# Optimization experiments

Measured on AMD Instinct MI355X. Metric: run time of the kernel, lower is better.

The kernel has to match this reference:

```python
import jax, jax.numpy as jnp
import numpy as np

NEG_INF = float(np.finfo(np.float32).min)
B, KLEN, QLEN, KDIM, QDIM, ADIM, H = 2, 2048, 2048, 512, 512, 512, 8
D_K = ADIM // H


def setup_inputs() -> dict:
    key = jax.random.key(0)
    ks = jax.random.split(key, 12)
    s = 0.05  # param init scale
    inp = {
        "key_in": jax.random.normal(ks[0], (B, KLEN, KDIM), jnp.float32),
        "value_in": jax.random.normal(ks[1], (B, KLEN, KDIM), jnp.float32),
        "query_in": jax.random.normal(ks[2], (B, QLEN, QDIM), jnp.float32),
        "Wk": jax.random.normal(ks[3], (KDIM, ADIM), jnp.float32) * s,
        "bk": jax.random.normal(ks[4], (ADIM,), jnp.float32) * s,
        "Wv": jax.random.normal(ks[5], (KDIM, ADIM), jnp.float32) * s,
        "bv": jax.random.normal(ks[6], (ADIM,), jnp.float32) * s,
        "Wq": jax.random.normal(ks[7], (QDIM, ADIM), jnp.float32) * s,
        "bq": jax.random.normal(ks[8], (ADIM,), jnp.float32) * s,
        "Wo": jax.random.normal(ks[9], (ADIM, KDIM), jnp.float32) * s,
        "bo": jax.random.normal(ks[10], (KDIM,), jnp.float32) * s,
    }
    # key-length padding mask, [B, qlen, klen]; 0 = masked
    klens = jnp.array([KLEN, KLEN - 512], jnp.int32)
    valid = (jnp.arange(KLEN)[None, :] < klens[:, None]).astype(jnp.int32)  # [B, klen]
    inp["mask"] = jnp.broadcast_to(valid[:, None, :], (B, QLEN, KLEN))
    return inp


def reference(key_in, value_in, query_in, Wk, bk, Wv, bv, Wq, bq, Wo, bo, mask):
    # projections -> [B, L, H, d_k]
    k = (key_in @ Wk + bk).reshape(B, KLEN, H, D_K)
    v = (value_in @ Wv + bv).reshape(B, KLEN, H, D_K)
    q = (query_in @ Wq + bq).reshape(B, QLEN, H, D_K)
    # scaled dot-product scores [B, H, qlen, klen]
    e = jnp.einsum('bqhd,bkhd->bhqk', q, k) / jnp.sqrt(jnp.float32(D_K))
    e = jnp.where(mask[:, None, :, :] == 0, NEG_INF, e)
    aw = jax.nn.softmax(e, axis=-1)  # dropout p=0.0 -> identity
    cv = jnp.einsum('bhqk,bkhd->bqhd', aw, v).reshape(B, QLEN, ADIM)
    cv = cv @ Wo + bo  # [B, qlen, kdim]
    return cv, aw
```

## Files before the change

kernel.cpp:

```cpp
#include <hip/hip_runtime.h>

typedef short sh8 __attribute__((ext_vector_type(8)));
typedef float fx4 __attribute__((ext_vector_type(4)));
typedef float fl4 __attribute__((ext_vector_type(4)));
typedef unsigned short us4 __attribute__((ext_vector_type(4)));

__device__ __forceinline__ unsigned short f2bf(float f) {
    union { float f; unsigned u; } v; v.f = f;
    unsigned r = v.u + 0x7FFFu + ((v.u >> 16) & 1u);
    return (unsigned short)(r >> 16);
}
__device__ __forceinline__ unsigned pk2(float a, float b) {
    return (unsigned)f2bf(a) | ((unsigned)f2bf(b) << 16);
}
__device__ __forceinline__ void gl16(const unsigned short* g, unsigned short* l) {
    __builtin_amdgcn_global_load_lds(
        (const __attribute__((address_space(1))) unsigned int*)g,
        (__attribute__((address_space(3))) unsigned int*)l, 16, 0, 0);
}

__global__ __launch_bounds__(256) void prep(const float* __restrict__ w0,
                                            const float* __restrict__ w1,
                                            const float* __restrict__ w2,
                                            const float* __restrict__ w3,
                                            const int* __restrict__ mask,
                                            unsigned short* __restrict__ wt,
                                            unsigned long long* __restrict__ mp2) {
    __shared__ float tw[32][33];
    const int bid = blockIdx.x, tid = threadIdx.x;
    if (bid < 1024) {
        const int t = bid;
        const int z = t >> 8, bx = t & 15, by = (t >> 4) & 15;
        const float* W = z == 0 ? w0 : z == 1 ? w1 : z == 2 ? w2 : w3;
        unsigned short* Wt = wt + (size_t)z * 262144;
        const int tx = tid & 31, ty = tid >> 5;
        #pragma unroll
        for (int i = 0; i < 4; ++i)
            tw[ty + i * 8][tx] = W[(size_t)(by * 32 + ty + i * 8) * 512 + bx * 32 + tx];
        __syncthreads();
        #pragma unroll
        for (int i = 0; i < 4; ++i)
            Wt[(size_t)(bx * 32 + ty + i * 8) * 512 + by * 32 + tx] = f2bf(tw[tx][ty + i * 8]);
    } else {
        const int p = bid - 1024;
        const int b = p >> 3, k = (p & 7) * 256 + tid;
        int v = mask[(size_t)b * 4194304 + k];
        unsigned long long bal = __ballot(v != 0);
        if ((tid & 63) == 0) mp2[b * 32 + (k >> 6)] = bal;
    }
}

template <int MODE>
__global__ __launch_bounds__(256) void gemm_k(const unsigned short* __restrict__ Abf,
                                              const float* __restrict__ xk,
                                              const float* __restrict__ xv,
                                              const float* __restrict__ xq,
                                              const unsigned short* __restrict__ Wtall,
                                              const float* __restrict__ b0,
                                              const float* __restrict__ b1,
                                              const float* __restrict__ b2,
                                              void* __restrict__ outp,
                                              unsigned short* __restrict__ VtB) {
    const int z = blockIdx.z;
    const float* Afp = (MODE == 0) ? (z == 0 ? xk : (z == 1 ? xv : xq)) : nullptr;
    const unsigned short* Bt = Wtall + (size_t)z * (512 * 512);
    const float* bias = (MODE == 0) ? (z == 0 ? b0 : (z == 1 ? b1 : b2)) : b0;

    __shared__ __align__(16) unsigned short As[128 * 64];
    __shared__ __align__(16) unsigned short Bs[64 * 64];

    const int tid = threadIdx.x;
    const int wid = tid >> 6, lane = tid & 63, lr = lane & 15, lg = lane >> 4;
    const int wr = wid >> 1, wc = wid & 1;
    const int mblk = blockIdx.x * 128, nblk = blockIdx.y * 64;
    const int r7 = lr & 7;

    fx4 acc[4][2];
    #pragma unroll
    for (int mf = 0; mf < 4; ++mf)
        #pragma unroll
        for (int nf = 0; nf < 2; ++nf)
            #pragma unroll
            for (int j = 0; j < 4; ++j) acc[mf][nf][j] = 0.f;

    for (int kt = 0; kt < 8; ++kt) {
        __syncthreads();
        if (MODE == 0) {
            #pragma unroll
            for (int g = 0; g < 4; ++g) {
                int ci = g * 256 + tid;
                int r = ci >> 3, c = ci & 7;
                const float* src = Afp + (size_t)(mblk + r) * 512 + kt * 64 + c * 8;
                float4 v0 = *(const float4*)(src);
                float4 v1 = *(const float4*)(src + 4);
                union { unsigned short u[8]; sh8 v; } pk;
                pk.u[0] = f2bf(v0.x); pk.u[1] = f2bf(v0.y);
                pk.u[2] = f2bf(v0.z); pk.u[3] = f2bf(v0.w);
                pk.u[4] = f2bf(v1.x); pk.u[5] = f2bf(v1.y);
                pk.u[6] = f2bf(v1.z); pk.u[7] = f2bf(v1.w);
                *(sh8*)&As[r * 64 + ((c ^ (r & 7)) * 8)] = pk.v;
            }
        } else {
            #pragma unroll
            for (int g = 0; g < 4; ++g) {
                int ci = wid * 256 + g * 64 + lane;
                int r = ci >> 3, c = (ci & 7) ^ (r & 7);
                gl16(Abf + (size_t)(mblk + r) * 512 + kt * 64 + c * 8, &As[(wid * 256 + g * 64) * 8]);
            }
        }
        #pragma unroll
        for (int g = 0; g < 2; ++g) {
            int ci = wid * 128 + g * 64 + lane;
            int r = ci >> 3, c = (ci & 7) ^ (r & 7);
            gl16(Bt + (size_t)(nblk + r) * 512 + kt * 64 + c * 8, &Bs[(wid * 128 + g * 64) * 8]);
        }
        __syncthreads();
        #pragma unroll
        for (int d = 0; d < 2; ++d) {
            sh8 af[4], bf[2];
            #pragma unroll
            for (int mf = 0; mf < 4; ++mf)
                af[mf] = *(const sh8*)&As[(wr * 64 + mf * 16 + lr) * 64 + (((d * 4 + lg) ^ r7) * 8)];
            #pragma unroll
            for (int nf = 0; nf < 2; ++nf)
                bf[nf] = *(const sh8*)&Bs[(wc * 32 + nf * 16 + lr) * 64 + (((d * 4 + lg) ^ r7) * 8)];
            #pragma unroll
            for (int mf = 0; mf < 4; ++mf)
                #pragma unroll
                for (int nf = 0; nf < 2; ++nf)
                    acc[mf][nf] = __builtin_amdgcn_mfma_f32_16x16x32_bf16(af[mf], bf[nf], acc[mf][nf], 0, 0, 0);
        }
    }

    if (MODE == 0 && z == 1) {
        #pragma unroll
        for (int nf = 0; nf < 2; ++nf) {
            int n = nblk + wc * 32 + nf * 16 + lr;
            float bv = bias[n];
            int h = n >> 6, dd = n & 63;
            #pragma unroll
            for (int mf = 0; mf < 4; ++mf) {
                int m0 = mblk + wr * 64 + mf * 16 + lg * 4;
                int bb = m0 >> 11, lq = m0 & 2047;
                ushort4 o;
                o.x = f2bf(acc[mf][nf][0] + bv);
                o.y = f2bf(acc[mf][nf][1] + bv);
                o.z = f2bf(acc[mf][nf][2] + bv);
                o.w = f2bf(acc[mf][nf][3] + bv);
                *(ushort4*)(VtB + ((size_t)(bb * 8 + h) * 64 + dd) * 2048 + lq) = o;
            }
        }
    } else {
        #pragma unroll
        for (int nf = 0; nf < 2; ++nf) {
            int n = nblk + wc * 32 + nf * 16 + lr;
            float bv = bias[n];
            #pragma unroll
            for (int mf = 0; mf < 4; ++mf) {
                #pragma unroll
                for (int j = 0; j < 4; ++j) {
                    int m = mblk + wr * 64 + mf * 16 + lg * 4 + j;
                    float val = acc[mf][nf][j] + bv;
                    if (MODE == 0) {
                        if (z == 2) val *= 0.125f;
                        int bb = m >> 11, lq = m & 2047, h = n >> 6, dd = n & 63;
                        ((unsigned short*)outp)[(size_t)(((z * 2 + bb) * 8 + h) * 2048 + lq) * 64 + dd] = f2bf(val);
                    } else {
                        ((float*)outp)[(size_t)m * 512 + n] = val;
                    }
                }
            }
        }
    }
}

__device__ __forceinline__ void stage_k1(const unsigned short* Kg, unsigned short* sK,
                                         int t, int w, int lane) {
    #pragma unroll
    for (int g = 0; g < 2; ++g) {
        int ci = w * 128 + g * 64 + lane;
        int r = ci >> 3, c = (ci & 7) ^ (r & 7);
        gl16(Kg + (size_t)(t * 64 + r) * 64 + c * 8, sK + (w * 128 + g * 64) * 8);
    }
}
__device__ __forceinline__ void stage_kv(const unsigned short* Kg, const unsigned short* Vg,
                                         unsigned short* sK, unsigned short* sV,
                                         int t, int w, int lane) {
    #pragma unroll
    for (int g = 0; g < 2; ++g) {
        int ci = w * 128 + g * 64 + lane;
        int r = ci >> 3, c = (ci & 7) ^ (r & 7);
        gl16(Kg + (size_t)(t * 64 + r) * 64 + c * 8, sK + (w * 128 + g * 64) * 8);
        gl16(Vg + (size_t)r * 2048 + t * 64 + c * 8, sV + (w * 128 + g * 64) * 8);
    }
}

__global__ __launch_bounds__(256, 2) void attn_fused(const unsigned short* __restrict__ qkv,
                                                     const unsigned short* __restrict__ Vt,
                                                     const unsigned long long* __restrict__ mp2,
                                                     float* __restrict__ aw,
                                                     unsigned short* __restrict__ cv) {
    const int bid = blockIdx.x;
    const int swz = (bid & 7) * 64 + (bid >> 3);
    const int qb = swz & 31, bh = swz >> 5;
    const int b = bh >> 3, h = bh & 7;
    const unsigned short* Kg = qkv + (size_t)bh * 131072;
    const unsigned short* Vg = Vt + (size_t)bh * 131072;
    const unsigned short* Qg = qkv + 2 * 2097152 + (size_t)bh * 131072 + (size_t)qb * 4096;

    __shared__ __align__(16) unsigned short Ks[2][4096];
    __shared__ __align__(16) unsigned short Vs[2][4096];
    __shared__ __align__(16) unsigned short Pb[4096];

    const int tid = threadIdx.x, w = tid >> 6, lane = tid & 63, lr = lane & 15, lg = lane >> 4;
    const int r7 = lr & 7;
    const int q = qb * 64 + w * 16 + lr;

    sh8 qf0 = *(const sh8*)(Qg + (w * 16 + lr) * 64 + lg * 8);
    sh8 qf1 = *(const sh8*)(Qg + (w * 16 + lr) * 64 + 32 + lg * 8);
    unsigned long long mwv = (lane < 32) ? mp2[b * 32 + lane] : 0ull;

    float m_ = -3e38f, l_ = 0.f;
    asm volatile("s_waitcnt vmcnt(0)" ::: "memory");
    stage_k1(Kg, Ks[0], 0, w, lane);
    stage_k1(Kg, Ks[1], 1, w, lane);
    for (int kt = 0; kt < 32; ++kt) {
        if (kt >= 1 && kt <= 30)
            stage_k1(Kg, Ks[(kt + 1) & 1], kt + 1, w, lane);
        if (kt == 31) asm volatile("s_waitcnt vmcnt(0)" ::: "memory");
        else          asm volatile("s_waitcnt vmcnt(2)" ::: "memory");
        asm volatile("s_barrier" ::: "memory");
        unsigned long long mw = __shfl(mwv, kt, 64);
        if (mw != 0ull) {
            const unsigned short* KsB = Ks[kt & 1];
            fx4 accs[4];
            #pragma unroll
            for (int mt = 0; mt < 4; ++mt) {
                sh8 kf0 = *(const sh8*)&KsB[(mt * 16 + lr) * 64 + ((lg ^ r7) * 8)];
                sh8 kf1 = *(const sh8*)&KsB[(mt * 16 + lr) * 64 + (((4 + lg) ^ r7) * 8)];
                fx4 zz; zz[0] = 0.f; zz[1] = 0.f; zz[2] = 0.f; zz[3] = 0.f;
                zz = __builtin_amdgcn_mfma_f32_16x16x32_bf16(kf0, qf0, zz, 0, 0, 0);
                accs[mt] = __builtin_amdgcn_mfma_f32_16x16x32_bf16(kf1, qf1, zz, 0, 0, 0);
            }
            float sv[16], tmax = -3e38f;
            if (mw == ~0ull) {
                #pragma unroll
                for (int mt = 0; mt < 4; ++mt)
                    #pragma unroll
                    for (int j = 0; j < 4; ++j) {
                        float s = accs[mt][j];
                        sv[mt * 4 + j] = s; tmax = fmaxf(tmax, s);
                    }
            } else {
                #pragma unroll
                for (int mt = 0; mt < 4; ++mt)
                    #pragma unroll
                    for (int j = 0; j < 4; ++j) {
                        int kl = mt * 16 + lg * 4 + j;
                        bool ok = (mw >> kl) & 1ull;
                        float s = ok ? accs[mt][j] : -3e38f;
                        sv[mt * 4 + j] = s; tmax = fmaxf(tmax, s);
                    }
            }
            float mnew = fmaxf(m_, tmax);
            float ps = 0.f;
            #pragma unroll
            for (int i = 0; i < 16; ++i) ps += __expf(sv[i] - mnew);
            l_ = l_ * __expf(m_ - mnew) + ps;
            m_ = mnew;
        }
        asm volatile("s_barrier" ::: "memory");
    }
    #pragma unroll
    for (int off = 16; off <= 32; off <<= 1) {
        float mo = __shfl_xor(m_, off), lo = __shfl_xor(l_, off);
        float mn = fmaxf(m_, mo);
        l_ = l_ * __expf(m_ - mn) + lo * __expf(mo - mn);
        m_ = mn;
    }
    const float M = (l_ > 0.f) ? m_ : 0.f;
    const float rinv = (l_ > 0.f) ? 1.f / l_ : 0.f;

    fx4 acco[4];
    #pragma unroll
    for (int md = 0; md < 4; ++md) { acco[md][0] = 0.f; acco[md][1] = 0.f; acco[md][2] = 0.f; acco[md][3] = 0.f; }
    float* awb = aw + (size_t)bh * 4194304 + (size_t)q * 2048;

    asm volatile("s_waitcnt vmcnt(0)" ::: "memory");
    stage_kv(Kg, Vg, Ks[0], Vs[0], 0, w, lane);
    stage_kv(Kg, Vg, Ks[1], Vs[1], 1, w, lane);

    for (int kt = 0; kt < 32; ++kt) {
        if (kt >= 1 && kt <= 30)
            stage_kv(Kg, Vg, Ks[(kt + 1) & 1], Vs[(kt + 1) & 1], kt + 1, w, lane);
        if (kt == 0 || kt == 31) asm volatile("s_waitcnt vmcnt(4)" ::: "memory");
        else                     asm volatile("s_waitcnt vmcnt(8)" ::: "memory");
        asm volatile("s_barrier" ::: "memory");

        unsigned long long mw = __shfl(mwv, kt, 64);
        const unsigned short* KsB = Ks[kt & 1];
        const unsigned short* VsB = Vs[kt & 1];

        if (mw != 0ull) {
            fx4 accs[4];
            #pragma unroll
            for (int mt = 0; mt < 4; ++mt) {
                sh8 kf0 = *(const sh8*)&KsB[(mt * 16 + lr) * 64 + ((lg ^ r7) * 8)];
                sh8 kf1 = *(const sh8*)&KsB[(mt * 16 + lr) * 64 + (((4 + lg) ^ r7) * 8)];
                fx4 zz; zz[0] = 0.f; zz[1] = 0.f; zz[2] = 0.f; zz[3] = 0.f;
                zz = __builtin_amdgcn_mfma_f32_16x16x32_bf16(kf0, qf0, zz, 0, 0, 0);
                accs[mt] = __builtin_amdgcn_mfma_f32_16x16x32_bf16(kf1, qf1, zz, 0, 0, 0);
            }
            bool full = (mw == ~0ull);
            #pragma unroll
            for (int mt = 0; mt < 4; ++mt) {
                fl4 pw;
                #pragma unroll
                for (int j = 0; j < 4; ++j) {
                    int kl = mt * 16 + lg * 4 + j;
                    bool ok = full || ((mw >> kl) & 1ull);
                    float p = ok ? __expf(accs[mt][j] - M) * rinv : 0.f;
                    pw[j] = p;
                }
                __builtin_nontemporal_store(pw, (fl4*)(awb + kt * 64 + mt * 16 + lg * 4));
                int sc = (mt * 2 + (lg >> 1)) ^ r7;
                *(uint2*)&Pb[(w * 16 + lr) * 64 + sc * 8 + (lg & 1) * 4] =
                    make_uint2(pk2(pw[0], pw[1]), pk2(pw[2], pw[3]));
            }
            asm volatile("s_waitcnt lgkmcnt(0)" ::: "memory");
            __builtin_amdgcn_sched_barrier(0);
            sh8 bp0 = *(const sh8*)&Pb[(w * 16 + lr) * 64 + ((lg ^ r7) * 8)];
            sh8 bp1 = *(const sh8*)&Pb[(w * 16 + lr) * 64 + (((4 + lg) ^ r7) * 8)];
            #pragma unroll
            for (int md = 0; md < 4; ++md) {
                sh8 vf0 = *(const sh8*)&VsB[(md * 16 + lr) * 64 + ((lg ^ r7) * 8)];
                sh8 vf1 = *(const sh8*)&VsB[(md * 16 + lr) * 64 + (((4 + lg) ^ r7) * 8)];
                acco[md] = __builtin_amdgcn_mfma_f32_16x16x32_bf16(vf0, bp0, acco[md], 0, 0, 0);
                acco[md] = __builtin_amdgcn_mfma_f32_16x16x32_bf16(vf1, bp1, acco[md], 0, 0, 0);
            }
        } else {
            fl4 z4 = {0.f, 0.f, 0.f, 0.f};
            #pragma unroll
            for (int mt = 0; mt < 4; ++mt)
                __builtin_nontemporal_store(z4, (fl4*)(awb + kt * 64 + mt * 16 + lg * 4));
        }
        asm volatile("s_barrier" ::: "memory");
    }

    #pragma unroll
    for (int md = 0; md < 4; ++md) {
        us4 o;
        o[0] = f2bf(acco[md][0]); o[1] = f2bf(acco[md][1]);
        o[2] = f2bf(acco[md][2]); o[3] = f2bf(acco[md][3]);
        __builtin_nontemporal_store(o,
            (us4*)(cv + (size_t)(b * 2048 + q) * 512 + h * 64 + md * 16 + lg * 4));
    }
}

extern "C" void kernel_launch(void* const* d_in, const int* in_sizes, int n_in,
                              void* d_out, int out_size, void* d_ws, size_t ws_size,
                              hipStream_t stream) {
    const float* key_in   = (const float*)d_in[0];
    const float* value_in = (const float*)d_in[1];
    const float* query_in = (const float*)d_in[2];
    const float* Wk = (const float*)d_in[3];
    const float* bk = (const float*)d_in[4];
    const float* Wv = (const float*)d_in[5];
    const float* bv = (const float*)d_in[6];
    const float* Wq = (const float*)d_in[7];
    const float* bq = (const float*)d_in[8];
    const float* Wo = (const float*)d_in[9];
    const float* bo = (const float*)d_in[10];
    const int* mask = (const int*)d_in[11];

    char* ws = (char*)d_ws;
    unsigned short* qkv   = (unsigned short*)(ws);
    unsigned short* cvb   = (unsigned short*)(ws + 4194304);
    unsigned short* wt    = (unsigned short*)(ws + 12582912);
    unsigned short* VtB   = (unsigned short*)(ws + 14680064);
    unsigned long long* mp2 = (unsigned long long*)(ws + 18874368);

    float* out_cv = (float*)d_out;
    float* out_aw = (float*)d_out + 2097152;

    prep<<<dim3(1040), 256, 0, stream>>>(Wk, Wv, Wq, Wo, mask, wt, mp2);
    gemm_k<0><<<dim3(32, 8, 3), 256, 0, stream>>>(nullptr, key_in, value_in, query_in,
                                                  wt, bk, bv, bq, qkv, VtB);
    attn_fused<<<dim3(512), 256, 0, stream>>>(qkv, VtB, mp2, out_aw, cvb);
    gemm_k<1><<<dim3(32, 8, 1), 256, 0, stream>>>(cvb, nullptr, nullptr, nullptr,
                                                  wt + 3 * 262144, bo, bo, bo, out_cv, (unsigned short*)nullptr);
}
```

Measured before the change: 146.4 us.

## Use exp2 softmax with folded log2e scale, async fp32 A loads, hardware bf16 packing

The query scale now folds in log2(e), so softmax uses native exp2. The normalisation is folded into the exponent as m + log2(l), which removes the multiply by the reciprocal. The projection GEMM now loads fp32 activations straight into LDS with global_load_lds and converts them to bf16 at fragment load with v_cvt_pk_bf16_f32, replacing the register-side conversion. Nontemporal stores on the attention-weight and context outputs become plain stores, and bf16 packing uses the hardware instruction throughout. The cost is double the LDS for the fp32 A tile and conversion work repeated per fragment read.

After: 127.4 us. -13.0%, faster.

```diff
diff --git a/kernel.cpp b/kernel.cpp
--- a/kernel.cpp
+++ b/kernel.cpp
@@ -10,10 +10,13 @@
     unsigned r = v.u + 0x7FFFu + ((v.u >> 16) & 1u);
     return (unsigned short)(r >> 16);
 }
-__device__ __forceinline__ unsigned pk2(float a, float b) {
-    return (unsigned)f2bf(a) | ((unsigned)f2bf(b) << 16);
-}
-__device__ __forceinline__ void gl16(const unsigned short* g, unsigned short* l) {
+__device__ __forceinline__ float EX2(float x) { return __builtin_amdgcn_exp2f(x); }
+__device__ __forceinline__ unsigned cvtpk(float a, float b) {
+    unsigned r;
+    asm("v_cvt_pk_bf16_f32 %0, %1, %2" : "=v"(r) : "v"(a), "v"(b));
+    return r;
+}
+__device__ __forceinline__ void gl16(const void* g, void* l) {
     __builtin_amdgcn_global_load_lds(
         (const __attribute__((address_space(1))) unsigned int*)g,
         (__attribute__((address_space(3))) unsigned int*)l, 16, 0, 0);
@@ -66,8 +69,10 @@
     const unsigned short* Bt = Wtall + (size_t)z * (512 * 512);
     const float* bias = (MODE == 0) ? (z == 0 ? b0 : (z == 1 ? b1 : b2)) : b0;
 
-    __shared__ __align__(16) unsigned short As[128 * 64];
+    __shared__ __align__(16) char AsRaw[MODE == 0 ? 32768 : 16384];
     __shared__ __align__(16) unsigned short Bs[64 * 64];
+    float* Asf = (float*)AsRaw;
+    unsigned short* Asb = (unsigned short*)AsRaw;
 
     const int tid = threadIdx.x;
     const int wid = tid >> 6, lane = tid & 63, lr = lane & 15, lg = lane >> 4;
@@ -87,25 +92,19 @@
         __syncthreads();
         if (MODE == 0) {
             #pragma unroll
-            for (int g = 0; g < 4; ++g) {
-                int ci = g * 256 + tid;
-                int r = ci >> 3, c = ci & 7;
-                const float* src = Afp + (size_t)(mblk + r) * 512 + kt * 64 + c * 8;
-                float4 v0 = *(const float4*)(src);
-                float4 v1 = *(const float4*)(src + 4);
-                union { unsigned short u[8]; sh8 v; } pk;
-                pk.u[0] = f2bf(v0.x); pk.u[1] = f2bf(v0.y);
-                pk.u[2] = f2bf(v0.z); pk.u[3] = f2bf(v0.w);
-                pk.u[4] = f2bf(v1.x); pk.u[5] = f2bf(v1.y);
-                pk.u[6] = f2bf(v1.z); pk.u[7] = f2bf(v1.w);
-                *(sh8*)&As[r * 64 + ((c ^ (r & 7)) * 8)] = pk.v;
+            for (int g = 0; g < 8; ++g) {
+                int ci = wid * 512 + g * 64 + lane;
+                int r = ci >> 4, c = (ci & 15) ^ (r & 15);
+                gl16(Afp + (size_t)(mblk + r) * 512 + kt * 64 + c * 4,
+                     &Asf[(wid * 512 + g * 64) * 4]);
             }
         } else {
             #pragma unroll
             for (int g = 0; g < 4; ++g) {
                 int ci = wid * 256 + g * 64 + lane;
                 int r = ci >> 3, c = (ci & 7) ^ (r & 7);
-                gl16(Abf + (size_t)(mblk + r) * 512 + kt * 64 + c * 8, &As[(wid * 256 + g * 64) * 8]);
+                gl16(Abf + (size_t)(mblk + r) * 512 + kt * 64 + c * 8,
+                     &Asb[(wid * 256 + g * 64) * 8]);
             }
         }
         #pragma unroll
@@ -119,8 +118,20 @@
         for (int d = 0; d < 2; ++d) {
             sh8 af[4], bf[2];
             #pragma unroll
-            for (int mf = 0; mf < 4; ++mf)
-                af[mf] = *(const sh8*)&As[(wr * 64 + mf * 16 + lr) * 64 + (((d * 4 + lg) ^ r7) * 8)];
+            for (int mf = 0; mf < 4; ++mf) {
+                if (MODE == 0) {
+                    int R = wr * 64 + mf * 16 + lr;
+                    int j0 = (d * 4 + lg) * 2;
+                    fl4 a0 = *(const fl4*)&Asf[R * 64 + ((j0 ^ (R & 15)) << 2)];
+                    fl4 a1 = *(const fl4*)&Asf[R * 64 + (((j0 + 1) ^ (R & 15)) << 2)];
+                    union { unsigned u[4]; sh8 v; } cc;
+                    cc.u[0] = cvtpk(a0[0], a0[1]); cc.u[1] = cvtpk(a0[2], a0[3]);
+                    cc.u[2] = cvtpk(a1[0], a1[1]); cc.u[3] = cvtpk(a1[2], a1[3]);
+                    af[mf] = cc.v;
+                } else {
+                    af[mf] = *(const sh8*)&Asb[(wr * 64 + mf * 16 + lr) * 64 + (((d * 4 + lg) ^ r7) * 8)];
+                }
+            }
             #pragma unroll
             for (int nf = 0; nf < 2; ++nf)
                 bf[nf] = *(const sh8*)&Bs[(wc * 32 + nf * 16 + lr) * 64 + (((d * 4 + lg) ^ r7) * 8)];
@@ -162,7 +173,7 @@
                     int m = mblk + wr * 64 + mf * 16 + lg * 4 + j;
                     float val = acc[mf][nf][j] + bv;
                     if (MODE == 0) {
-                        if (z == 2) val *= 0.125f;
+                        if (z == 2) val *= 0.180336880f;
                         int bb = m >> 11, lq = m & 2047, h = n >> 6, dd = n & 63;
                         ((unsigned short*)outp)[(size_t)(((z * 2 + bb) * 8 + h) * 2048 + lq) * 64 + dd] = f2bf(val);
                     } else {
@@ -265,8 +276,8 @@
             float mnew = fmaxf(m_, tmax);
             float ps = 0.f;
             #pragma unroll
-            for (int i = 0; i < 16; ++i) ps += __expf(sv[i] - mnew);
-            l_ = l_ * __expf(m_ - mnew) + ps;
+            for (int i = 0; i < 16; ++i) ps += EX2(sv[i] - mnew);
+            l_ = l_ * EX2(m_ - mnew) + ps;
             m_ = mnew;
         }
         asm volatile("s_barrier" ::: "memory");
@@ -275,11 +286,10 @@
     for (int off = 16; off <= 32; off <<= 1) {
         float mo = __shfl_xor(m_, off), lo = __shfl_xor(l_, off);
         float mn = fmaxf(m_, mo);
-        l_ = l_ * __expf(m_ - mn) + lo * __expf(mo - mn);
+        l_ = l_ * EX2(m_ - mn) + lo * EX2(mo - mn);
         m_ = mn;
     }
-    const float M = (l_ > 0.f) ? m_ : 0.f;
-    const float rinv = (l_ > 0.f) ? 1.f / l_ : 0.f;
+    const float Mshift = (l_ > 0.f) ? (m_ + __log2f(l_)) : 3e38f;
 
     fx4 acco[4];
     #pragma unroll
@@ -319,13 +329,12 @@
                 for (int j = 0; j < 4; ++j) {
                     int kl = mt * 16 + lg * 4 + j;
                     bool ok = full || ((mw >> kl) & 1ull);
-                    float p = ok ? __expf(accs[mt][j] - M) * rinv : 0.f;
-                    pw[j] = p;
+                    pw[j] = EX2((ok ? accs[mt][j] : -3e38f) - Mshift);
                 }
-                __builtin_nontemporal_store(pw, (fl4*)(awb + kt * 64 + mt * 16 + lg * 4));
+                *(fl4*)(awb + kt * 64 + mt * 16 + lg * 4) = pw;
                 int sc = (mt * 2 + (lg >> 1)) ^ r7;
                 *(uint2*)&Pb[(w * 16 + lr) * 64 + sc * 8 + (lg & 1) * 4] =
-                    make_uint2(pk2(pw[0], pw[1]), pk2(pw[2], pw[3]));
+                    make_uint2(cvtpk(pw[0], pw[1]), cvtpk(pw[2], pw[3]));
             }
             asm volatile("s_waitcnt lgkmcnt(0)" ::: "memory");
             __builtin_amdgcn_sched_barrier(0);
@@ -342,18 +351,15 @@
             fl4 z4 = {0.f, 0.f, 0.f, 0.f};
             #pragma unroll
             for (int mt = 0; mt < 4; ++mt)
-                __builtin_nontemporal_store(z4, (fl4*)(awb + kt * 64 + mt * 16 + lg * 4));
+                *(fl4*)(awb + kt * 64 + mt * 16 + lg * 4) = z4;
         }
         asm volatile("s_barrier" ::: "memory");
     }
 
     #pragma unroll
     for (int md = 0; md < 4; ++md) {
-        us4 o;
-        o[0] = f2bf(acco[md][0]); o[1] = f2bf(acco[md][1]);
-        o[2] = f2bf(acco[md][2]); o[3] = f2bf(acco[md][3]);
-        __builtin_nontemporal_store(o,
-            (us4*)(cv + (size_t)(b * 2048 + q) * 512 + h * 64 + md * 16 + lg * 4));
+        uint2 o = make_uint2(cvtpk(acco[md][0], acco[md][1]), cvtpk(acco[md][2], acco[md][3]));
+        *(uint2*)(cv + (size_t)(b * 2048 + q) * 512 + h * 64 + md * 16 + lg * 4) = o;
     }
 }
 
```
